# Kernel optimization log

Measured on AMD Instinct MI355X. Metric: run time of the kernel, lower is better.

Reference implementation:

```python
import jax, jax.numpy as jnp
import numpy as np

INPUT_SIZE = 1024
HEAD_SIZE = 64


def setup_inputs() -> dict:
    key = jax.random.key(0)
    kx, kk, kq, kv = jax.random.split(key, 4)
    B, T, C, H = 4, 4096, INPUT_SIZE, HEAD_SIZE
    x = jax.random.normal(kx, (B, T, C), dtype=jnp.float32)
    # nn.Linear(C, H, bias=False) weight is (H, C); we store transposed (C, H)
    # so that y = x @ W matches torch's x @ weight.T
    scale = 1.0 / np.sqrt(C)
    Wk = jax.random.uniform(kk, (C, H), dtype=jnp.float32, minval=-scale, maxval=scale)
    Wq = jax.random.uniform(kq, (C, H), dtype=jnp.float32, minval=-scale, maxval=scale)
    Wv = jax.random.uniform(kv, (C, H), dtype=jnp.float32, minval=-scale, maxval=scale)
    return {"x": x, "Wk": Wk, "Wq": Wq, "Wv": Wv}


def reference(x, Wk, Wq, Wv):
    B, T, C = x.shape
    k = x @ Wk  # (B, T, H)
    q = x @ Wq
    v = x @ Wv
    H = k.shape[-1]
    # scaled scores (B, T, T)
    wei = jnp.einsum('bth,bsh->bts', q, k) * (H ** -0.5)
    causal = jnp.tril(jnp.ones((T, T), dtype=bool))
    wei = jnp.where(causal, wei, -jnp.inf)
    wei = jax.nn.softmax(wei, axis=-1)
    out = jnp.einsum('bts,bsh->bth', wei, v)  # (B, T, H)
    return out
```

## Files before the change

### kernel.cpp

```cpp
#include <hip/hip_runtime.h>
#include <math.h>


#define BT   16384
#define TDIM 4096
#define CDIM 1024
#define HDIM 64
#define ACCW 68

typedef __attribute__((ext_vector_type(8))) short bf16x8;
typedef __attribute__((ext_vector_type(4))) float f32x4;
typedef __attribute__((ext_vector_type(8))) unsigned short us8;
typedef __attribute__((ext_vector_type(4))) unsigned short us4;

static __device__ __forceinline__ unsigned short f2bf(float f) {
    unsigned int u = __float_as_uint(f);
    u += 0x7fffu + ((u >> 16) & 1u);
    return (unsigned short)(u >> 16);
}

static __device__ __forceinline__ void pswap(unsigned &x, unsigned &y) {
    asm("v_permlane32_swap_b32 %0, %1" : "+v"(x), "+v"(y));
    asm("v_permlane16_swap_b32 %0, %1" : "+v"(x), "+v"(y));
}

__global__ __launch_bounds__(256) void wtrans_zero(
    const float* __restrict__ Wk, const float* __restrict__ Wq,
    const float* __restrict__ Wv, unsigned short* __restrict__ wtg,
    float* __restrict__ accp)
{
    int idx = blockIdx.x * 256 + threadIdx.x;
    int mat = idx >> 16;
    int rem = idx & 65535;
    int h = rem >> 10, c = rem & 1023;
    const float* W = (mat == 0) ? Wk : (mat == 1) ? Wq : Wv;
    wtg[idx] = f2bf(W[c * HDIM + h]);
    for (int i = idx; i < BT * ACCW; i += 196608) accp[i] = 0.f;
}

__global__ __launch_bounds__(512) void qkv_proj(
    const float* __restrict__ x, const unsigned short* __restrict__ wtg,
    unsigned short* __restrict__ kg, unsigned short* __restrict__ qg,
    unsigned short* __restrict__ vtg)
{
    __shared__ __align__(16) unsigned short xs[32][72];
    __shared__ __align__(16) unsigned short wts[192][72];
    const int t = threadIdx.x;
    const int lane = t & 63, wv = t >> 6, quad = lane >> 4, l16 = lane & 15;
    const int mt = wv >> 2;
    const int nq = wv & 3;
    const int row0 = blockIdx.x * 32;

    const int xr = t >> 4, xc4 = (t & 15) * 4;
    const int wn = t >> 3, wc8 = (t & 7) * 8;

    f32x4 acc3[3];
    #pragma unroll
    for (int i = 0; i < 3; i++) acc3[i] = (f32x4){0.f, 0.f, 0.f, 0.f};

    float4 xv = *(const float4*)&x[(size_t)(row0 + xr) * CDIM + xc4];
    us8 w0 = *(const us8*)&wtg[(size_t)(wn +   0) * CDIM + wc8];
    us8 w1 = *(const us8*)&wtg[(size_t)(wn +  64) * CDIM + wc8];
    us8 w2 = *(const us8*)&wtg[(size_t)(wn + 128) * CDIM + wc8];

    for (int cc = 0; cc < CDIM; cc += 64) {
        __syncthreads();
        us4 pk = { f2bf(xv.x), f2bf(xv.y), f2bf(xv.z), f2bf(xv.w) };
        *(us4*)&xs[xr][xc4] = pk;
        *(us8*)&wts[wn +   0][wc8] = w0;
        *(us8*)&wts[wn +  64][wc8] = w1;
        *(us8*)&wts[wn + 128][wc8] = w2;
        __syncthreads();
        if (cc + 64 < CDIM) {
            int nc = cc + 64;
            xv = *(const float4*)&x[(size_t)(row0 + xr) * CDIM + nc + xc4];
            w0 = *(const us8*)&wtg[(size_t)(wn +   0) * CDIM + nc + wc8];
            w1 = *(const us8*)&wtg[(size_t)(wn +  64) * CDIM + nc + wc8];
            w2 = *(const us8*)&wtg[(size_t)(wn + 128) * CDIM + nc + wc8];
        }
        bf16x8 a0 = *(const bf16x8*)&xs[mt * 16 + l16][quad * 8];
        bf16x8 a1 = *(const bf16x8*)&xs[mt * 16 + l16][32 + quad * 8];
        #pragma unroll
        for (int j = 0; j < 3; j++) {
            int nt = nq * 3 + j;
            bf16x8 b0 = *(const bf16x8*)&wts[nt * 16 + l16][quad * 8];
            bf16x8 b1 = *(const bf16x8*)&wts[nt * 16 + l16][32 + quad * 8];
            acc3[j] = __builtin_amdgcn_mfma_f32_16x16x32_bf16(a0, b0, acc3[j], 0, 0, 0);
            acc3[j] = __builtin_amdgcn_mfma_f32_16x16x32_bf16(a1, b1, acc3[j], 0, 0, 0);
        }
    }

    const int mrow = row0 + mt * 16 + quad * 4;
    #pragma unroll
    for (int j = 0; j < 3; j++) {
        int nt = nq * 3 + j;
        int mat = nt >> 2;
        int col = (nt & 3) * 16 + l16;
        if (mat == 2) {
            int bb = mrow >> 12, tr = mrow & 4095;
            us4 pv = { f2bf(acc3[j][0]), f2bf(acc3[j][1]),
                       f2bf(acc3[j][2]), f2bf(acc3[j][3]) };
            *(us4*)&vtg[((size_t)(bb * HDIM + col) << 12) + tr] = pv;
        } else {
            float s = (mat == 1) ? 0.125f : 1.0f;
            unsigned short* dst = (mat == 0) ? kg : qg;
            #pragma unroll
            for (int reg = 0; reg < 4; reg++)
                dst[(size_t)(mrow + reg) * HDIM + col] = f2bf(acc3[j][reg] * s);
        }
    }
}

__global__ __launch_bounds__(256) void attn(
    const unsigned short* __restrict__ qg, const unsigned short* __restrict__ kg,
    const unsigned short* __restrict__ vtg, float* __restrict__ accp)
{
    __shared__ __align__(16) unsigned short Ks[64][72];
    __shared__ __align__(16) unsigned short Vt[80][72];

    const int t = threadIdx.x;
    const int lane = t & 63, wv = t >> 6, quad = lane >> 4, l16 = lane & 15;

    const int b = blockIdx.x / 160;
    const int s = blockIdx.x - b * 160;
    int qt, c;
    if (s < 16)      { qt = s;               c = 0; }
    else if (s < 48) { int u = s - 16; qt = 16 + (u >> 1); c = u & 1; }
    else if (s < 96) { int u = s - 48; int q3 = u / 3; qt = 32 + q3; c = u - 3 * q3; }
    else             { int u = s - 96; qt = 48 + (u >> 2); c = u & 3; }

    const size_t bbase = (size_t)b * TDIM;
    const int Q0 = qt * 64;
    const int kt0 = c * 16;
    const int kt1 = (kt0 + 15 < qt) ? kt0 + 15 : qt;

    for (int i = t; i < 16 * 72; i += 256) {
        int r = i / 72, cc = i - r * 72;
        Vt[64 + r][cc] = (r == 0) ? (unsigned short)0x3F80 : (unsigned short)0;
    }

    const int qrow = Q0 + wv * 16 + l16;
    bf16x8 qa0 = *(const bf16x8*)&qg[(bbase + qrow) * HDIM + quad * 8];
    bf16x8 qa1 = *(const bf16x8*)&qg[(bbase + qrow) * HDIM + 32 + quad * 8];

    f32x4 O[5];
    #pragma unroll
    for (int i = 0; i < 5; i++) O[i] = (f32x4){0.f, 0.f, 0.f, 0.f};

    const int fr = t >> 3, fc = (t & 7) * 8;

    us8 kr0 = *(const us8*)&kg[(bbase + kt0 * 64 + fr) * HDIM + fc];
    us8 kr1 = *(const us8*)&kg[(bbase + kt0 * 64 + fr + 32) * HDIM + fc];
    us8 vr0 = *(const us8*)&vtg[((size_t)(b * HDIM + fr) << 12) + kt0 * 64 + fc];
    us8 vr1 = *(const us8*)&vtg[((size_t)(b * HDIM + fr + 32) << 12) + kt0 * 64 + fc];

    const int qloc = wv * 16 + l16;
    for (int kt = kt0; kt <= kt1; kt++) {
        __syncthreads();
        *(us8*)&Ks[fr][fc] = kr0;
        *(us8*)&Ks[fr + 32][fc] = kr1;
        *(us8*)&Vt[fr][fc] = vr0;
        *(us8*)&Vt[fr + 32][fc] = vr1;
        __syncthreads();
        if (kt < kt1) {
            int kn = kt + 1;
            kr0 = *(const us8*)&kg[(bbase + kn * 64 + fr) * HDIM + fc];
            kr1 = *(const us8*)&kg[(bbase + kn * 64 + fr + 32) * HDIM + fc];
            vr0 = *(const us8*)&vtg[((size_t)(b * HDIM + fr) << 12) + kn * 64 + fc];
            vr1 = *(const us8*)&vtg[((size_t)(b * HDIM + fr + 32) << 12) + kn * 64 + fc];
        }

        f32x4 sT[4];
        #pragma unroll
        for (int st = 0; st < 4; st++) {
            bf16x8 kb0 = *(const bf16x8*)&Ks[st * 16 + l16][quad * 8];
            bf16x8 kb1 = *(const bf16x8*)&Ks[st * 16 + l16][32 + quad * 8];
            f32x4 z = (f32x4){0.f, 0.f, 0.f, 0.f};
            z = __builtin_amdgcn_mfma_f32_16x16x32_bf16(kb0, qa0, z, 0, 0, 0);
            z = __builtin_amdgcn_mfma_f32_16x16x32_bf16(kb1, qa1, z, 0, 0, 0);
            sT[st] = z;
        }

        const bool diag = (kt == qt);
        float p[4][4];
        #pragma unroll
        for (int st = 0; st < 4; st++) {
            #pragma unroll
            for (int r = 0; r < 4; r++) {
                int kkloc = st * 16 + quad * 4 + r;
                p[st][r] = (diag && (kkloc > qloc)) ? 0.f : __expf(sT[st][r]);
            }
        }

        unsigned cpk[4][2];
        #pragma unroll
        for (int st = 0; st < 4; st++) {
            asm("v_cvt_pk_bf16_f32 %0, %1, %2"
                : "=v"(cpk[st][0]) : "v"(p[st][0]), "v"(p[st][1]));
            asm("v_cvt_pk_bf16_f32 %0, %1, %2"
                : "=v"(cpk[st][1]) : "v"(p[st][2]), "v"(p[st][3]));
        }
        union { unsigned u[4]; bf16x8 v; } pa0u, pa1u;
        {
            unsigned a0 = cpk[0][0], b0 = cpk[1][0]; pswap(a0, b0);
            unsigned a1 = cpk[0][1], b1 = cpk[1][1]; pswap(a1, b1);
            pa0u.u[0] = a0; pa0u.u[1] = a1; pa0u.u[2] = b0; pa0u.u[3] = b1;
            unsigned a2 = cpk[2][0], b2 = cpk[3][0]; pswap(a2, b2);
            unsigned a3 = cpk[2][1], b3 = cpk[3][1]; pswap(a3, b3);
            pa1u.u[0] = a2; pa1u.u[1] = a3; pa1u.u[2] = b2; pa1u.u[3] = b3;
        }
        const bf16x8 pa0 = pa0u.v, pa1 = pa1u.v;

        #pragma unroll
        for (int nt = 0; nt < 5; nt++) {
            bf16x8 vb0 = *(const bf16x8*)&Vt[nt * 16 + l16][quad * 8];
            bf16x8 vb1 = *(const bf16x8*)&Vt[nt * 16 + l16][32 + quad * 8];
            O[nt] = __builtin_amdgcn_mfma_f32_16x16x32_bf16(pa0, vb0, O[nt], 0, 0, 0);
            O[nt] = __builtin_amdgcn_mfma_f32_16x16x32_bf16(pa1, vb1, O[nt], 0, 0, 0);
        }
    }

    const int grow = (b << 12) + Q0 + wv * 16 + quad * 4;
    #pragma unroll
    for (int nt = 0; nt < 4; nt++)
        #pragma unroll
        for (int r = 0; r < 4; r++)
            atomicAdd(&accp[(size_t)(grow + r) * ACCW + nt * 16 + l16], O[nt][r]);
    if (l16 == 0) {
        #pragma unroll
        for (int r = 0; r < 4; r++)
            atomicAdd(&accp[(size_t)(grow + r) * ACCW + 64], O[4][r]);
    }
}

__global__ __launch_bounds__(256) void normalize(
    const float* __restrict__ accp, float* __restrict__ out)
{
    int idx = blockIdx.x * 256 + threadIdx.x;
    int row = idx >> 4, c4 = (idx & 15) * 4;
    float inv = 1.f / accp[(size_t)row * ACCW + 64];
    float4 o = *(const float4*)&accp[(size_t)row * ACCW + c4];
    float4 res = make_float4(o.x * inv, o.y * inv, o.z * inv, o.w * inv);
    *(float4*)&out[(size_t)row * HDIM + c4] = res;
}

extern "C" void kernel_launch(void* const* d_in, const int* in_sizes, int n_in,
                              void* d_out, int out_size, void* d_ws, size_t ws_size,
                              hipStream_t stream) {
    const float* x  = (const float*)d_in[0];
    const float* Wk = (const float*)d_in[1];
    const float* Wq = (const float*)d_in[2];
    const float* Wv = (const float*)d_in[3];
    float* out = (float*)d_out;

    unsigned short* wtg = (unsigned short*)d_ws;
    unsigned short* kg  = wtg + 196608;
    unsigned short* qg  = kg + (size_t)BT * HDIM;
    unsigned short* vtg = qg + (size_t)BT * HDIM;
    float* accp = (float*)(vtg + (size_t)4 * HDIM * TDIM);

    wtrans_zero<<<768, 256, 0, stream>>>(Wk, Wq, Wv, wtg, accp);
    qkv_proj<<<BT / 32, 512, 0, stream>>>(x, wtg, kg, qg, vtg);
    attn<<<4 * 160, 256, 0, stream>>>(qg, kg, vtg, accp);
    normalize<<<BT * HDIM / (4 * 256), 256, 0, stream>>>(accp, out);
}
```

Before: 144.1 us.

## Read K/V and weights directly from global memory instead of LDS staging

```diff
diff --git a/kernel.cpp b/kernel.cpp
--- a/kernel.cpp
+++ b/kernel.cpp
@@ -43,51 +43,49 @@
     unsigned short* __restrict__ kg, unsigned short* __restrict__ qg,
     unsigned short* __restrict__ vtg)
 {
-    __shared__ __align__(16) unsigned short xs[32][72];
-    __shared__ __align__(16) unsigned short wts[192][72];
+    __shared__ __align__(16) unsigned short xs[2][32][72];
     const int t = threadIdx.x;
     const int lane = t & 63, wv = t >> 6, quad = lane >> 4, l16 = lane & 15;
     const int mt = wv >> 2;
     const int nq = wv & 3;
     const int row0 = blockIdx.x * 32;
-
     const int xr = t >> 4, xc4 = (t & 15) * 4;
-    const int wn = t >> 3, wc8 = (t & 7) * 8;
 
     f32x4 acc3[3];
     #pragma unroll
     for (int i = 0; i < 3; i++) acc3[i] = (f32x4){0.f, 0.f, 0.f, 0.f};
 
-    float4 xv = *(const float4*)&x[(size_t)(row0 + xr) * CDIM + xc4];
-    us8 w0 = *(const us8*)&wtg[(size_t)(wn +   0) * CDIM + wc8];
-    us8 w1 = *(const us8*)&wtg[(size_t)(wn +  64) * CDIM + wc8];
-    us8 w2 = *(const us8*)&wtg[(size_t)(wn + 128) * CDIM + wc8];
-
-    for (int cc = 0; cc < CDIM; cc += 64) {
-        __syncthreads();
+    const size_t xrow = (size_t)(row0 + xr) * CDIM + xc4;
+
+    float4 xv = *(const float4*)&x[xrow];
+    {
         us4 pk = { f2bf(xv.x), f2bf(xv.y), f2bf(xv.z), f2bf(xv.w) };
-        *(us4*)&xs[xr][xc4] = pk;
-        *(us8*)&wts[wn +   0][wc8] = w0;
-        *(us8*)&wts[wn +  64][wc8] = w1;
-        *(us8*)&wts[wn + 128][wc8] = w2;
-        __syncthreads();
-        if (cc + 64 < CDIM) {
-            int nc = cc + 64;
-            xv = *(const float4*)&x[(size_t)(row0 + xr) * CDIM + nc + xc4];
-            w0 = *(const us8*)&wtg[(size_t)(wn +   0) * CDIM + nc + wc8];
-            w1 = *(const us8*)&wtg[(size_t)(wn +  64) * CDIM + nc + wc8];
-            w2 = *(const us8*)&wtg[(size_t)(wn + 128) * CDIM + nc + wc8];
-        }
-        bf16x8 a0 = *(const bf16x8*)&xs[mt * 16 + l16][quad * 8];
-        bf16x8 a1 = *(const bf16x8*)&xs[mt * 16 + l16][32 + quad * 8];
+        *(us4*)&xs[0][xr][xc4] = pk;
+    }
+    xv = *(const float4*)&x[xrow + 64];
+    __syncthreads();
+
+    for (int it = 0; it < 16; it++) {
+        const int buf = it & 1;
+        if (it + 1 < 16) {
+            us4 pk = { f2bf(xv.x), f2bf(xv.y), f2bf(xv.z), f2bf(xv.w) };
+            *(us4*)&xs[buf ^ 1][xr][xc4] = pk;
+            if (it + 2 < 16)
+                xv = *(const float4*)&x[xrow + (it + 2) * 64];
+        }
+        const int cc = it * 64;
+        bf16x8 a0 = *(const bf16x8*)&xs[buf][mt * 16 + l16][quad * 8];
+        bf16x8 a1 = *(const bf16x8*)&xs[buf][mt * 16 + l16][32 + quad * 8];
         #pragma unroll
         for (int j = 0; j < 3; j++) {
             int nt = nq * 3 + j;
-            bf16x8 b0 = *(const bf16x8*)&wts[nt * 16 + l16][quad * 8];
-            bf16x8 b1 = *(const bf16x8*)&wts[nt * 16 + l16][32 + quad * 8];
+            const unsigned short* wr = &wtg[(size_t)(nt * 16 + l16) * CDIM + cc];
+            bf16x8 b0 = *(const bf16x8*)&wr[quad * 8];
+            bf16x8 b1 = *(const bf16x8*)&wr[32 + quad * 8];
             acc3[j] = __builtin_amdgcn_mfma_f32_16x16x32_bf16(a0, b0, acc3[j], 0, 0, 0);
             acc3[j] = __builtin_amdgcn_mfma_f32_16x16x32_bf16(a1, b1, acc3[j], 0, 0, 0);
         }
+        __syncthreads();
     }
 
     const int mrow = row0 + mt * 16 + quad * 4;
@@ -115,9 +113,6 @@
     const unsigned short* __restrict__ qg, const unsigned short* __restrict__ kg,
     const unsigned short* __restrict__ vtg, float* __restrict__ accp)
 {
-    __shared__ __align__(16) unsigned short Ks[64][72];
-    __shared__ __align__(16) unsigned short Vt[80][72];
-
     const int t = threadIdx.x;
     const int lane = t & 63, wv = t >> 6, quad = lane >> 4, l16 = lane & 15;
 
@@ -134,62 +129,50 @@
     const int kt0 = c * 16;
     const int kt1 = (kt0 + 15 < qt) ? kt0 + 15 : qt;
 
-    for (int i = t; i < 16 * 72; i += 256) {
-        int r = i / 72, cc = i - r * 72;
-        Vt[64 + r][cc] = (r == 0) ? (unsigned short)0x3F80 : (unsigned short)0;
-    }
-
     const int qrow = Q0 + wv * 16 + l16;
-    bf16x8 qa0 = *(const bf16x8*)&qg[(bbase + qrow) * HDIM + quad * 8];
-    bf16x8 qa1 = *(const bf16x8*)&qg[(bbase + qrow) * HDIM + 32 + quad * 8];
+    const bf16x8 qa0 = *(const bf16x8*)&qg[(bbase + qrow) * HDIM + quad * 8];
+    const bf16x8 qa1 = *(const bf16x8*)&qg[(bbase + qrow) * HDIM + 32 + quad * 8];
+
+    const short onev = (l16 == 0) ? (short)0x3F80 : (short)0;
+    const bf16x8 ones = { onev, onev, onev, onev, onev, onev, onev, onev };
 
     f32x4 O[5];
     #pragma unroll
     for (int i = 0; i < 5; i++) O[i] = (f32x4){0.f, 0.f, 0.f, 0.f};
 
-    const int fr = t >> 3, fc = (t & 7) * 8;
-
-    us8 kr0 = *(const us8*)&kg[(bbase + kt0 * 64 + fr) * HDIM + fc];
-    us8 kr1 = *(const us8*)&kg[(bbase + kt0 * 64 + fr + 32) * HDIM + fc];
-    us8 vr0 = *(const us8*)&vtg[((size_t)(b * HDIM + fr) << 12) + kt0 * 64 + fc];
-    us8 vr1 = *(const us8*)&vtg[((size_t)(b * HDIM + fr + 32) << 12) + kt0 * 64 + fc];
+    const unsigned short* kB = kg + bbase * HDIM;
+    const unsigned short* vB = vtg + ((size_t)(b * HDIM) << 12);
 
     const int qloc = wv * 16 + l16;
     for (int kt = kt0; kt <= kt1; kt++) {
-        __syncthreads();
-        *(us8*)&Ks[fr][fc] = kr0;
-        *(us8*)&Ks[fr + 32][fc] = kr1;
-        *(us8*)&Vt[fr][fc] = vr0;
-        *(us8*)&Vt[fr + 32][fc] = vr1;
-        __syncthreads();
-        if (kt < kt1) {
-            int kn = kt + 1;
-            kr0 = *(const us8*)&kg[(bbase + kn * 64 + fr) * HDIM + fc];
-            kr1 = *(const us8*)&kg[(bbase + kn * 64 + fr + 32) * HDIM + fc];
-            vr0 = *(const us8*)&vtg[((size_t)(b * HDIM + fr) << 12) + kn * 64 + fc];
-            vr1 = *(const us8*)&vtg[((size_t)(b * HDIM + fr + 32) << 12) + kn * 64 + fc];
-        }
-
+        const unsigned short* kp = kB + (size_t)(kt * 64) * HDIM;
         f32x4 sT[4];
         #pragma unroll
         for (int st = 0; st < 4; st++) {
-            bf16x8 kb0 = *(const bf16x8*)&Ks[st * 16 + l16][quad * 8];
-            bf16x8 kb1 = *(const bf16x8*)&Ks[st * 16 + l16][32 + quad * 8];
+            const unsigned short* kr = kp + (size_t)(st * 16 + l16) * HDIM;
+            bf16x8 kb0 = *(const bf16x8*)&kr[quad * 8];
+            bf16x8 kb1 = *(const bf16x8*)&kr[32 + quad * 8];
             f32x4 z = (f32x4){0.f, 0.f, 0.f, 0.f};
             z = __builtin_amdgcn_mfma_f32_16x16x32_bf16(kb0, qa0, z, 0, 0, 0);
             z = __builtin_amdgcn_mfma_f32_16x16x32_bf16(kb1, qa1, z, 0, 0, 0);
             sT[st] = z;
         }
 
-        const bool diag = (kt == qt);
         float p[4][4];
-        #pragma unroll
-        for (int st = 0; st < 4; st++) {
+        if (kt == qt) {
             #pragma unroll
-            for (int r = 0; r < 4; r++) {
-                int kkloc = st * 16 + quad * 4 + r;
-                p[st][r] = (diag && (kkloc > qloc)) ? 0.f : __expf(sT[st][r]);
-            }
+            for (int st = 0; st < 4; st++)
+                #pragma unroll
+                for (int r = 0; r < 4; r++) {
+                    int kkloc = st * 16 + quad * 4 + r;
+                    p[st][r] = (kkloc > qloc) ? 0.f : __expf(sT[st][r]);
+                }
+        } else {
+            #pragma unroll
+            for (int st = 0; st < 4; st++)
+                #pragma unroll
+                for (int r = 0; r < 4; r++)
+                    p[st][r] = __expf(sT[st][r]);
         }
 
         unsigned cpk[4][2];
@@ -212,12 +195,15 @@
         const bf16x8 pa0 = pa0u.v, pa1 = pa1u.v;
 
         #pragma unroll
-        for (int nt = 0; nt < 5; nt++) {
-            bf16x8 vb0 = *(const bf16x8*)&Vt[nt * 16 + l16][quad * 8];
-            bf16x8 vb1 = *(const bf16x8*)&Vt[nt * 16 + l16][32 + quad * 8];
+        for (int nt = 0; nt < 4; nt++) {
+            const unsigned short* vr = vB + ((size_t)(nt * 16 + l16) << 12) + kt * 64;
+            bf16x8 vb0 = *(const bf16x8*)&vr[quad * 8];
+            bf16x8 vb1 = *(const bf16x8*)&vr[32 + quad * 8];
             O[nt] = __builtin_amdgcn_mfma_f32_16x16x32_bf16(pa0, vb0, O[nt], 0, 0, 0);
             O[nt] = __builtin_amdgcn_mfma_f32_16x16x32_bf16(pa1, vb1, O[nt], 0, 0, 0);
         }
+        O[4] = __builtin_amdgcn_mfma_f32_16x16x32_bf16(pa0, ones, O[4], 0, 0, 0);
+        O[4] = __builtin_amdgcn_mfma_f32_16x16x32_bf16(pa1, ones, O[4], 0, 0, 0);
     }
 
     const int grow = (b << 12) + Q0 + wv * 16 + quad * 4;
```

New measurement: 227.8 us. +58.2%, slower.
